# Kernel optimization log

Measured on AMD Instinct MI355X. Metric: run time of the kernel, lower is better.

## Reference

```python
import jax, jax.numpy as jnp
import numpy as np


def setup_inputs() -> dict:
    key = jax.random.key(0)
    kq, kk, kv = jax.random.split(key, 3)
    B, d, N = 8, 768, 6144
    q = jax.random.normal(kq, (B, d, N), dtype=jnp.float32)
    k = jax.random.normal(kk, (B, d, N), dtype=jnp.float32)
    v = jax.random.normal(kv, (B, d, N), dtype=jnp.float32)
    return {"q": q, "k": k, "v": v, "head_dim": 32, "kernel_size": 3}


def reference(q, k, v, head_dim, kernel_size):
    B, d, N = q.shape
    h = d // head_dim          # number of heads
    g = N // kernel_size       # number of local windows
    scale = head_dim ** (-0.5)
    # [B, d, N] -> [B, h, head_dim, ks, g] -> attention layout
    qr = q.reshape(B, h, head_dim, kernel_size, g).transpose(0, 1, 4, 3, 2)  # [B,h,g,ks,hd]
    kr = k.reshape(B, h, head_dim, kernel_size, g).transpose(0, 1, 4, 2, 3)  # [B,h,g,hd,ks]
    vr = v.reshape(B, h, head_dim, kernel_size, g).transpose(0, 1, 4, 3, 2)  # [B,h,g,ks,hd]
    attn = jnp.einsum('bhgkd,bhgdj->bhgkj', qr, kr) * scale                   # [B,h,g,ks,ks]
    attn = jax.nn.softmax(attn, axis=-1)
    x = jnp.einsum('bhgkj,bhgjd->bhgkd', attn, vr)                            # [B,h,g,ks,hd]
    # transpose(1,2) then reshape(B, N, d): [B,g,h,ks,hd] -> [B,N,d]
    return x.transpose(0, 2, 1, 3, 4).reshape(B, N, d)
```

## Files before the change

### kernel.cpp

```cpp
#include <hip/hip_runtime.h>
#include <stdint.h>

constexpr int CB = 8;
constexpr int CD = 768;
constexpr int CN = 6144;
constexpr int HD = 32;
constexpr int KS = 3;
constexpr int CH = CD / HD;
constexpr int CG = CN / KS;

__global__ __launch_bounds__(256) void dilate_attn_kernel(
    const float* __restrict__ q, const float* __restrict__ k,
    const float* __restrict__ v, float* __restrict__ out) {
  const int tid   = blockIdx.x * 256 + threadIdx.x;
  const int lane  = threadIdx.x & 63;
  const int wav   = tid >> 6;
  const int slice = lane >> 4;
  const int wl    = lane & 15;
  const int gg    = (wav & 127) * 16 + wl;
  const int bh    = wav >> 7;
  const int hh    = bh % CH;
  const int b     = bh / CH;

  const uint32_t inoff = (uint32_t)(b * CD + hh * HD + slice * 8) * (uint32_t)CN
                       + (uint32_t)gg;

  float s00 = 0.f, s01 = 0.f, s02 = 0.f;
  float s10 = 0.f, s11 = 0.f, s12 = 0.f;
  float s20 = 0.f, s21 = 0.f, s22 = 0.f;
  #pragma unroll
  for (int d = 0; d < 8; ++d) {
    const uint32_t o = inoff + (uint32_t)d * CN;
    const float q0 = q[o], q1 = q[o + CG], q2 = q[o + 2 * CG];
    const float k0 = k[o], k1 = k[o + CG], k2 = k[o + 2 * CG];
    s00 = fmaf(q0, k0, s00); s01 = fmaf(q0, k1, s01); s02 = fmaf(q0, k2, s02);
    s10 = fmaf(q1, k0, s10); s11 = fmaf(q1, k1, s11); s12 = fmaf(q1, k2, s12);
    s20 = fmaf(q2, k0, s20); s21 = fmaf(q2, k1, s21); s22 = fmaf(q2, k2, s22);
  }

  float va[8], vb[8], vc[8];
  #pragma unroll
  for (int d = 0; d < 8; ++d) {
    const uint32_t o = inoff + (uint32_t)d * CN;
    va[d] = v[o]; vb[d] = v[o + CG]; vc[d] = v[o + 2 * CG];
  }

  s00 += __shfl_xor(s00, 16); s01 += __shfl_xor(s01, 16); s02 += __shfl_xor(s02, 16);
  s10 += __shfl_xor(s10, 16); s11 += __shfl_xor(s11, 16); s12 += __shfl_xor(s12, 16);
  s20 += __shfl_xor(s20, 16); s21 += __shfl_xor(s21, 16); s22 += __shfl_xor(s22, 16);
  s00 += __shfl_xor(s00, 32); s01 += __shfl_xor(s01, 32); s02 += __shfl_xor(s02, 32);
  s10 += __shfl_xor(s10, 32); s11 += __shfl_xor(s11, 32); s12 += __shfl_xor(s12, 32);
  s20 += __shfl_xor(s20, 32); s21 += __shfl_xor(s21, 32); s22 += __shfl_xor(s22, 32);

  const float scale = 0.17677669529663687f;
  {
    const float x0 = s00 * scale, x1 = s01 * scale, x2 = s02 * scale;
    const float m = fmaxf(fmaxf(x0, x1), x2);
    const float e0 = __expf(x0 - m), e1 = __expf(x1 - m), e2 = __expf(x2 - m);
    const float r = 1.f / (e0 + e1 + e2);
    s00 = e0 * r; s01 = e1 * r; s02 = e2 * r;
  }
  {
    const float x0 = s10 * scale, x1 = s11 * scale, x2 = s12 * scale;
    const float m = fmaxf(fmaxf(x0, x1), x2);
    const float e0 = __expf(x0 - m), e1 = __expf(x1 - m), e2 = __expf(x2 - m);
    const float r = 1.f / (e0 + e1 + e2);
    s10 = e0 * r; s11 = e1 * r; s12 = e2 * r;
  }
  {
    const float x0 = s20 * scale, x1 = s21 * scale, x2 = s22 * scale;
    const float m = fmaxf(fmaxf(x0, x1), x2);
    const float e0 = __expf(x0 - m), e1 = __expf(x1 - m), e2 = __expf(x2 - m);
    const float r = 1.f / (e0 + e1 + e2);
    s20 = e0 * r; s21 = e1 * r; s22 = e2 * r;
  }

  const uint32_t ooff = (uint32_t)(b * CG + gg) * (uint32_t)(CH * KS * HD)
                      + (uint32_t)(hh * KS * HD) + (uint32_t)(slice * 8);

  float o0, o1, o2, o3, o4, o5, o6, o7;
  o0 = fmaf(s00, va[0], fmaf(s01, vb[0], s02 * vc[0]));
  o1 = fmaf(s00, va[1], fmaf(s01, vb[1], s02 * vc[1]));
  o2 = fmaf(s00, va[2], fmaf(s01, vb[2], s02 * vc[2]));
  o3 = fmaf(s00, va[3], fmaf(s01, vb[3], s02 * vc[3]));
  o4 = fmaf(s00, va[4], fmaf(s01, vb[4], s02 * vc[4]));
  o5 = fmaf(s00, va[5], fmaf(s01, vb[5], s02 * vc[5]));
  o6 = fmaf(s00, va[6], fmaf(s01, vb[6], s02 * vc[6]));
  o7 = fmaf(s00, va[7], fmaf(s01, vb[7], s02 * vc[7]));
  *reinterpret_cast<float4*>(out + ooff + 0 * HD)     = make_float4(o0, o1, o2, o3);
  *reinterpret_cast<float4*>(out + ooff + 0 * HD + 4) = make_float4(o4, o5, o6, o7);
  o0 = fmaf(s10, va[0], fmaf(s11, vb[0], s12 * vc[0]));
  o1 = fmaf(s10, va[1], fmaf(s11, vb[1], s12 * vc[1]));
  o2 = fmaf(s10, va[2], fmaf(s11, vb[2], s12 * vc[2]));
  o3 = fmaf(s10, va[3], fmaf(s11, vb[3], s12 * vc[3]));
  o4 = fmaf(s10, va[4], fmaf(s11, vb[4], s12 * vc[4]));
  o5 = fmaf(s10, va[5], fmaf(s11, vb[5], s12 * vc[5]));
  o6 = fmaf(s10, va[6], fmaf(s11, vb[6], s12 * vc[6]));
  o7 = fmaf(s10, va[7], fmaf(s11, vb[7], s12 * vc[7]));
  *reinterpret_cast<float4*>(out + ooff + 1 * HD)     = make_float4(o0, o1, o2, o3);
  *reinterpret_cast<float4*>(out + ooff + 1 * HD + 4) = make_float4(o4, o5, o6, o7);
  o0 = fmaf(s20, va[0], fmaf(s21, vb[0], s22 * vc[0]));
  o1 = fmaf(s20, va[1], fmaf(s21, vb[1], s22 * vc[1]));
  o2 = fmaf(s20, va[2], fmaf(s21, vb[2], s22 * vc[2]));
  o3 = fmaf(s20, va[3], fmaf(s21, vb[3], s22 * vc[3]));
  o4 = fmaf(s20, va[4], fmaf(s21, vb[4], s22 * vc[4]));
  o5 = fmaf(s20, va[5], fmaf(s21, vb[5], s22 * vc[5]));
  o6 = fmaf(s20, va[6], fmaf(s21, vb[6], s22 * vc[6]));
  o7 = fmaf(s20, va[7], fmaf(s21, vb[7], s22 * vc[7]));
  *reinterpret_cast<float4*>(out + ooff + 2 * HD)     = make_float4(o0, o1, o2, o3);
  *reinterpret_cast<float4*>(out + ooff + 2 * HD + 4) = make_float4(o4, o5, o6, o7);
}

extern "C" void kernel_launch(void* const* d_in, const int* in_sizes, int n_in,
                              void* d_out, int out_size, void* d_ws, size_t ws_size,
                              hipStream_t stream) {
  const float* q = (const float*)d_in[0];
  const float* k = (const float*)d_in[1];
  const float* v = (const float*)d_in[2];
  float* out = (float*)d_out;

  const int total = CB * CH * CG * 4;
  const int blocks = total / 256;
  dilate_attn_kernel<<<blocks, 256, 0, stream>>>(q, k, v, out);
}
```

Before: 128.3 us.

## Make waves persistent over g-chunks with register double-buffered q/k prefetch

Each wavefront now loops over 8 consecutive 16-wide window chunks instead of handling one. It prefetches the next chunk's q and k into a second register buffer while computing the current one, and the grid shrinks to 768 blocks. The aim is to overlap load latency with compute and cut launch and scheduling overhead. In exchange it uses more registers and keeps fewer waves in flight, which can reduce memory-level parallelism in a bandwidth-bound kernel.

```diff
diff --git a/kernel.cpp b/kernel.cpp
--- a/kernel.cpp
+++ b/kernel.cpp
@@ -8,107 +8,136 @@
 constexpr int KS = 3;
 constexpr int CH = CD / HD;
 constexpr int CG = CN / KS;
+constexpr int OSTR = CH * KS * HD;
+constexpr int ITER = 8;
 
 __global__ __launch_bounds__(256) void dilate_attn_kernel(
     const float* __restrict__ q, const float* __restrict__ k,
     const float* __restrict__ v, float* __restrict__ out) {
   const int tid   = blockIdx.x * 256 + threadIdx.x;
   const int lane  = threadIdx.x & 63;
-  const int wav   = tid >> 6;
+  const int wv    = tid >> 6;
   const int slice = lane >> 4;
   const int wl    = lane & 15;
-  const int gg    = (wav & 127) * 16 + wl;
-  const int bh    = wav >> 7;
+  const int bh    = wv >> 4;
   const int hh    = bh % CH;
   const int b     = bh / CH;
+  const int gg0   = (wv & 15) * 128 + wl;
 
-  const uint32_t inoff = (uint32_t)(b * CD + hh * HD + slice * 8) * (uint32_t)CN
-                       + (uint32_t)gg;
+  uint32_t inoff = (uint32_t)(b * CD + hh * HD + slice * 8) * (uint32_t)CN
+                 + (uint32_t)gg0;
+  uint32_t ooff  = (uint32_t)(b * CG + gg0) * (uint32_t)OSTR
+                 + (uint32_t)(hh * KS * HD + slice * 8);
 
-  float s00 = 0.f, s01 = 0.f, s02 = 0.f;
-  float s10 = 0.f, s11 = 0.f, s12 = 0.f;
-  float s20 = 0.f, s21 = 0.f, s22 = 0.f;
+  float qr[2][24], kr[2][24];
+
   #pragma unroll
   for (int d = 0; d < 8; ++d) {
     const uint32_t o = inoff + (uint32_t)d * CN;
-    const float q0 = q[o], q1 = q[o + CG], q2 = q[o + 2 * CG];
-    const float k0 = k[o], k1 = k[o + CG], k2 = k[o + 2 * CG];
-    s00 = fmaf(q0, k0, s00); s01 = fmaf(q0, k1, s01); s02 = fmaf(q0, k2, s02);
-    s10 = fmaf(q1, k0, s10); s11 = fmaf(q1, k1, s11); s12 = fmaf(q1, k2, s12);
-    s20 = fmaf(q2, k0, s20); s21 = fmaf(q2, k1, s21); s22 = fmaf(q2, k2, s22);
+    qr[0][d] = q[o]; qr[0][8 + d] = q[o + CG]; qr[0][16 + d] = q[o + 2 * CG];
+    kr[0][d] = k[o]; kr[0][8 + d] = k[o + CG]; kr[0][16 + d] = k[o + 2 * CG];
   }
 
-  float va[8], vb[8], vc[8];
   #pragma unroll
-  for (int d = 0; d < 8; ++d) {
-    const uint32_t o = inoff + (uint32_t)d * CN;
-    va[d] = v[o]; vb[d] = v[o + CG]; vc[d] = v[o + 2 * CG];
+  for (int it = 0; it < ITER; ++it) {
+    const int cur = it & 1, nxt = cur ^ 1;
+
+    float va[8], vb2[8], vc2[8];
+    #pragma unroll
+    for (int d = 0; d < 8; ++d) {
+      const uint32_t o = inoff + (uint32_t)d * CN;
+      va[d] = v[o]; vb2[d] = v[o + CG]; vc2[d] = v[o + 2 * CG];
+    }
+
+    if (it + 1 < ITER) {
+      const uint32_t o1 = inoff + 16;
+      #pragma unroll
+      for (int d = 0; d < 8; ++d) {
+        const uint32_t o = o1 + (uint32_t)d * CN;
+        qr[nxt][d] = q[o]; qr[nxt][8 + d] = q[o + CG]; qr[nxt][16 + d] = q[o + 2 * CG];
+        kr[nxt][d] = k[o]; kr[nxt][8 + d] = k[o + CG]; kr[nxt][16 + d] = k[o + 2 * CG];
+      }
+    }
+
+    float s00 = 0.f, s01 = 0.f, s02 = 0.f;
+    float s10 = 0.f, s11 = 0.f, s12 = 0.f;
+    float s20 = 0.f, s21 = 0.f, s22 = 0.f;
+    #pragma unroll
+    for (int d = 0; d < 8; ++d) {
+      const float q0 = qr[cur][d], q1 = qr[cur][8 + d], q2 = qr[cur][16 + d];
+      const float k0 = kr[cur][d], k1 = kr[cur][8 + d], k2 = kr[cur][16 + d];
+      s00 = fmaf(q0, k0, s00); s01 = fmaf(q0, k1, s01); s02 = fmaf(q0, k2, s02);
+      s10 = fmaf(q1, k0, s10); s11 = fmaf(q1, k1, s11); s12 = fmaf(q1, k2, s12);
+      s20 = fmaf(q2, k0, s20); s21 = fmaf(q2, k1, s21); s22 = fmaf(q2, k2, s22);
+    }
+
+    s00 += __shfl_xor(s00, 16); s01 += __shfl_xor(s01, 16); s02 += __shfl_xor(s02, 16);
+    s10 += __shfl_xor(s10, 16); s11 += __shfl_xor(s11, 16); s12 += __shfl_xor(s12, 16);
+    s20 += __shfl_xor(s20, 16); s21 += __shfl_xor(s21, 16); s22 += __shfl_xor(s22, 16);
+    s00 += __shfl_xor(s00, 32); s01 += __shfl_xor(s01, 32); s02 += __shfl_xor(s02, 32);
+    s10 += __shfl_xor(s10, 32); s11 += __shfl_xor(s11, 32); s12 += __shfl_xor(s12, 32);
+    s20 += __shfl_xor(s20, 32); s21 += __shfl_xor(s21, 32); s22 += __shfl_xor(s22, 32);
+
+    const float scale = 0.17677669529663687f;
+    {
+      const float x0 = s00 * scale, x1 = s01 * scale, x2 = s02 * scale;
+      const float m = fmaxf(fmaxf(x0, x1), x2);
+      const float e0 = __expf(x0 - m), e1 = __expf(x1 - m), e2 = __expf(x2 - m);
+      const float r = 1.f / (e0 + e1 + e2);
+      s00 = e0 * r; s01 = e1 * r; s02 = e2 * r;
+    }
+    {
+      const float x0 = s10 * scale, x1 = s11 * scale, x2 = s12 * scale;
+      const float m = fmaxf(fmaxf(x0, x1), x2);
+      const float e0 = __expf(x0 - m), e1 = __expf(x1 - m), e2 = __expf(x2 - m);
+      const float r = 1.f / (e0 + e1 + e2);
+      s10 = e0 * r; s11 = e1 * r; s12 = e2 * r;
+    }
+    {
+      const float x0 = s20 * scale, x1 = s21 * scale, x2 = s22 * scale;
+      const float m = fmaxf(fmaxf(x0, x1), x2);
+      const float e0 = __expf(x0 - m), e1 = __expf(x1 - m), e2 = __expf(x2 - m);
+      const float r = 1.f / (e0 + e1 + e2);
+      s20 = e0 * r; s21 = e1 * r; s22 = e2 * r;
+    }
+
+    float o0, o1, o2, o3, o4, o5, o6, o7;
+    o0 = fmaf(s00, va[0], fmaf(s01, vb2[0], s02 * vc2[0]));
+    o1 = fmaf(s00, va[1], fmaf(s01, vb2[1], s02 * vc2[1]));
+    o2 = fmaf(s00, va[2], fmaf(s01, vb2[2], s02 * vc2[2]));
+    o3 = fmaf(s00, va[3], fmaf(s01, vb2[3], s02 * vc2[3]));
+    o4 = fmaf(s00, va[4], fmaf(s01, vb2[4], s02 * vc2[4]));
+    o5 = fmaf(s00, va[5], fmaf(s01, vb2[5], s02 * vc2[5]));
+    o6 = fmaf(s00, va[6], fmaf(s01, vb2[6], s02 * vc2[6]));
+    o7 = fmaf(s00, va[7], fmaf(s01, vb2[7], s02 * vc2[7]));
+    *reinterpret_cast<float4*>(out + ooff + 0 * HD)     = make_float4(o0, o1, o2, o3);
+    *reinterpret_cast<float4*>(out + ooff + 0 * HD + 4) = make_float4(o4, o5, o6, o7);
+
+    o0 = fmaf(s10, va[0], fmaf(s11, vb2[0], s12 * vc2[0]));
+    o1 = fmaf(s10, va[1], fmaf(s11, vb2[1], s12 * vc2[1]));
+    o2 = fmaf(s10, va[2], fmaf(s11, vb2[2], s12 * vc2[2]));
+    o3 = fmaf(s10, va[3], fmaf(s11, vb2[3], s12 * vc2[3]));
+    o4 = fmaf(s10, va[4], fmaf(s11, vb2[4], s12 * vc2[4]));
+    o5 = fmaf(s10, va[5], fmaf(s11, vb2[5], s12 * vc2[5]));
+    o6 = fmaf(s10, va[6], fmaf(s11, vb2[6], s12 * vc2[6]));
+    o7 = fmaf(s10, va[7], fmaf(s11, vb2[7], s12 * vc2[7]));
+    *reinterpret_cast<float4*>(out + ooff + 1 * HD)     = make_float4(o0, o1, o2, o3);
+    *reinterpret_cast<float4*>(out + ooff + 1 * HD + 4) = make_float4(o4, o5, o6, o7);
+
+    o0 = fmaf(s20, va[0], fmaf(s21, vb2[0], s22 * vc2[0]));
+    o1 = fmaf(s20, va[1], fmaf(s21, vb2[1], s22 * vc2[1]));
+    o2 = fmaf(s20, va[2], fmaf(s21, vb2[2], s22 * vc2[2]));
+    o3 = fmaf(s20, va[3], fmaf(s21, vb2[3], s22 * vc2[3]));
+    o4 = fmaf(s20, va[4], fmaf(s21, vb2[4], s22 * vc2[4]));
+    o5 = fmaf(s20, va[5], fmaf(s21, vb2[5], s22 * vc2[5]));
+    o6 = fmaf(s20, va[6], fmaf(s21, vb2[6], s22 * vc2[6]));
+    o7 = fmaf(s20, va[7], fmaf(s21, vb2[7], s22 * vc2[7]));
+    *reinterpret_cast<float4*>(out + ooff + 2 * HD)     = make_float4(o0, o1, o2, o3);
+    *reinterpret_cast<float4*>(out + ooff + 2 * HD + 4) = make_float4(o4, o5, o6, o7);
+
+    inoff += 16u;
+    ooff  += 16u * OSTR;
   }
-
-  s00 += __shfl_xor(s00, 16); s01 += __shfl_xor(s01, 16); s02 += __shfl_xor(s02, 16);
-  s10 += __shfl_xor(s10, 16); s11 += __shfl_xor(s11, 16); s12 += __shfl_xor(s12, 16);
-  s20 += __shfl_xor(s20, 16); s21 += __shfl_xor(s21, 16); s22 += __shfl_xor(s22, 16);
-  s00 += __shfl_xor(s00, 32); s01 += __shfl_xor(s01, 32); s02 += __shfl_xor(s02, 32);
-  s10 += __shfl_xor(s10, 32); s11 += __shfl_xor(s11, 32); s12 += __shfl_xor(s12, 32);
-  s20 += __shfl_xor(s20, 32); s21 += __shfl_xor(s21, 32); s22 += __shfl_xor(s22, 32);
-
-  const float scale = 0.17677669529663687f;
-  {
-    const float x0 = s00 * scale, x1 = s01 * scale, x2 = s02 * scale;
-    const float m = fmaxf(fmaxf(x0, x1), x2);
-    const float e0 = __expf(x0 - m), e1 = __expf(x1 - m), e2 = __expf(x2 - m);
-    const float r = 1.f / (e0 + e1 + e2);
-    s00 = e0 * r; s01 = e1 * r; s02 = e2 * r;
-  }
-  {
-    const float x0 = s10 * scale, x1 = s11 * scale, x2 = s12 * scale;
-    const float m = fmaxf(fmaxf(x0, x1), x2);
-    const float e0 = __expf(x0 - m), e1 = __expf(x1 - m), e2 = __expf(x2 - m);
-    const float r = 1.f / (e0 + e1 + e2);
-    s10 = e0 * r; s11 = e1 * r; s12 = e2 * r;
-  }
-  {
-    const float x0 = s20 * scale, x1 = s21 * scale, x2 = s22 * scale;
-    const float m = fmaxf(fmaxf(x0, x1), x2);
-    const float e0 = __expf(x0 - m), e1 = __expf(x1 - m), e2 = __expf(x2 - m);
-    const float r = 1.f / (e0 + e1 + e2);
-    s20 = e0 * r; s21 = e1 * r; s22 = e2 * r;
-  }
-
-  const uint32_t ooff = (uint32_t)(b * CG + gg) * (uint32_t)(CH * KS * HD)
-                      + (uint32_t)(hh * KS * HD) + (uint32_t)(slice * 8);
-
-  float o0, o1, o2, o3, o4, o5, o6, o7;
-  o0 = fmaf(s00, va[0], fmaf(s01, vb[0], s02 * vc[0]));
-  o1 = fmaf(s00, va[1], fmaf(s01, vb[1], s02 * vc[1]));
-  o2 = fmaf(s00, va[2], fmaf(s01, vb[2], s02 * vc[2]));
-  o3 = fmaf(s00, va[3], fmaf(s01, vb[3], s02 * vc[3]));
-  o4 = fmaf(s00, va[4], fmaf(s01, vb[4], s02 * vc[4]));
-  o5 = fmaf(s00, va[5], fmaf(s01, vb[5], s02 * vc[5]));
-  o6 = fmaf(s00, va[6], fmaf(s01, vb[6], s02 * vc[6]));
-  o7 = fmaf(s00, va[7], fmaf(s01, vb[7], s02 * vc[7]));
-  *reinterpret_cast<float4*>(out + ooff + 0 * HD)     = make_float4(o0, o1, o2, o3);
-  *reinterpret_cast<float4*>(out + ooff + 0 * HD + 4) = make_float4(o4, o5, o6, o7);
-  o0 = fmaf(s10, va[0], fmaf(s11, vb[0], s12 * vc[0]));
-  o1 = fmaf(s10, va[1], fmaf(s11, vb[1], s12 * vc[1]));
-  o2 = fmaf(s10, va[2], fmaf(s11, vb[2], s12 * vc[2]));
-  o3 = fmaf(s10, va[3], fmaf(s11, vb[3], s12 * vc[3]));
-  o4 = fmaf(s10, va[4], fmaf(s11, vb[4], s12 * vc[4]));
-  o5 = fmaf(s10, va[5], fmaf(s11, vb[5], s12 * vc[5]));
-  o6 = fmaf(s10, va[6], fmaf(s11, vb[6], s12 * vc[6]));
-  o7 = fmaf(s10, va[7], fmaf(s11, vb[7], s12 * vc[7]));
-  *reinterpret_cast<float4*>(out + ooff + 1 * HD)     = make_float4(o0, o1, o2, o3);
-  *reinterpret_cast<float4*>(out + ooff + 1 * HD + 4) = make_float4(o4, o5, o6, o7);
-  o0 = fmaf(s20, va[0], fmaf(s21, vb[0], s22 * vc[0]));
-  o1 = fmaf(s20, va[1], fmaf(s21, vb[1], s22 * vc[1]));
-  o2 = fmaf(s20, va[2], fmaf(s21, vb[2], s22 * vc[2]));
-  o3 = fmaf(s20, va[3], fmaf(s21, vb[3], s22 * vc[3]));
-  o4 = fmaf(s20, va[4], fmaf(s21, vb[4], s22 * vc[4]));
-  o5 = fmaf(s20, va[5], fmaf(s21, vb[5], s22 * vc[5]));
-  o6 = fmaf(s20, va[6], fmaf(s21, vb[6], s22 * vc[6]));
-  o7 = fmaf(s20, va[7], fmaf(s21, vb[7], s22 * vc[7]));
-  *reinterpret_cast<float4*>(out + ooff + 2 * HD)     = make_float4(o0, o1, o2, o3);
-  *reinterpret_cast<float4*>(out + ooff + 2 * HD + 4) = make_float4(o4, o5, o6, o7);
 }
 
 extern "C" void kernel_launch(void* const* d_in, const int* in_sizes, int n_in,
@@ -119,7 +148,6 @@
   const float* v = (const float*)d_in[2];
   float* out = (float*)d_out;
 
-  const int total = CB * CH * CG * 4;
-  const int blocks = total / 256;
+  const int blocks = 768;
   dilate_attn_kernel<<<blocks, 256, 0, stream>>>(q, k, v, out);
 }
```

After: 170.3 us. 32.8% more time.
